# Performance work log

Measured on AMD Instinct MI355X. Metric: run time of the kernel, lower is better.

## Reference

```python
import jax, jax.numpy as jnp
import numpy as np

EPS = 1e-12  # F.normalize eps
NEG_SLOPE = 0.2


def setup_inputs() -> dict:
    key = jax.random.key(0)
    ks = jax.random.split(key, 12)
    n_users, n_items, d, nnz, B = 100000, 100000, 64, 6400000, 4096
    N = n_users + n_items
    return {
        "rows": jax.random.randint(ks[0], (nnz,), 0, N, dtype=jnp.int32),
        "cols": jax.random.randint(ks[1], (nnz,), 0, N, dtype=jnp.int32),
        "vals": jax.random.uniform(ks[2], (nnz,), dtype=jnp.float32),
        "user_emb": jax.random.normal(ks[3], (n_users, d), dtype=jnp.float32),
        "item_emb": jax.random.normal(ks[4], (n_items, d), dtype=jnp.float32),
        "W_gc": jax.random.normal(ks[5], (3, d, d), dtype=jnp.float32) * 0.1,
        "b_gc": jax.random.normal(ks[6], (3, 1, d), dtype=jnp.float32) * 0.1,
        "W_bi": jax.random.normal(ks[7], (3, d, d), dtype=jnp.float32) * 0.1,
        "b_bi": jax.random.normal(ks[8], (3, 1, d), dtype=jnp.float32) * 0.1,
        "u": jax.random.randint(ks[9], (B,), 0, n_users, dtype=jnp.int32),
        "i": jax.random.randint(ks[10], (B,), 0, n_items, dtype=jnp.int32),
        "j": jax.random.randint(ks[11], (B,), 0, n_items, dtype=jnp.int32),
    }


def reference(rows, cols, vals, user_emb, item_emb, W_gc, b_gc, W_bi, b_bi, u, i, j):
    n_users = user_emb.shape[0]
    N = n_users + item_emb.shape[0]
    ego = jnp.concatenate([user_emb, item_emb], axis=0)  # [N, d]
    all_embeddings = [ego]
    for k in range(W_gc.shape[0]):
        # sparse adjacency SpMM: side[r] = sum_e vals[e] * ego[cols[e]] for rows[e]==r
        side = jax.ops.segment_sum(vals[:, None] * ego[cols], rows, num_segments=N)
        sum_emb = side @ W_gc[k] + b_gc[k]
        bi_emb = (ego * side) @ W_bi[k] + b_bi[k]
        ego = jax.nn.leaky_relu(sum_emb + bi_emb, negative_slope=NEG_SLOPE)
        # dropout p=0 (eval) -> identity; L2 normalize per node
        norm = jnp.linalg.norm(ego, axis=1, keepdims=True)
        all_embeddings.append(ego / jnp.maximum(norm, EPS))
    all_embeddings = jnp.concatenate(all_embeddings, axis=1)  # [N, d*(L+1)]
    u_g = all_embeddings[:n_users][u]
    i_g = all_embeddings[n_users:]
    return u_g, i_g[i], i_g[j]
```

## Files before the change

kernel.cpp:

```cpp
#include <hip/hip_runtime.h>
#include <hip/hip_bf16.h>

#define D 64
#define NEG_SLOPE 0.2f
#define EPS 1e-12f
#define CB 9
#define CROWS (1 << CB)
#define NBC_MAX 1024
#define TILE_E 8192

__device__ __forceinline__ unsigned short f32_to_bf16(float f) {
  unsigned b = __float_as_uint(f);
  return (unsigned short)((b + 0x7FFF + ((b >> 16) & 1)) >> 16);
}


__global__ __launch_bounds__(256) void hist_coarse(const int* __restrict__ rows,
                                                   int* __restrict__ bcount,
                                                   int nnz, int nbc) {
  __shared__ int h[NBC_MAX];
  for (int i = threadIdx.x; i < nbc; i += 256) h[i] = 0;
  __syncthreads();
  for (int k = blockIdx.x * 256 + threadIdx.x; k < nnz; k += gridDim.x * 256)
    atomicAdd(&h[rows[k] >> CB], 1);
  __syncthreads();
  for (int i = threadIdx.x; i < nbc; i += 256)
    if (h[i]) atomicAdd(&bcount[i], h[i]);
}

#define SCAN_E2 4
__global__ __launch_bounds__(256) void scan_buckets(
    const int* __restrict__ bcount, int* __restrict__ bbase,
    int* __restrict__ bcursor, int nbc, int nnz, int* __restrict__ row_ptr,
    int N) {
  __shared__ int sums[256];
  int base = threadIdx.x * SCAN_E2;
  int c[SCAN_E2];
  int tsum = 0;
#pragma unroll
  for (int i = 0; i < SCAN_E2; i++) {
    int idx = base + i;
    c[i] = (idx < nbc) ? bcount[idx] : 0;
    tsum += c[i];
  }
  sums[threadIdx.x] = tsum;
  __syncthreads();
  for (int off = 1; off < 256; off <<= 1) {
    int t = (threadIdx.x >= off) ? sums[threadIdx.x - off] : 0;
    __syncthreads();
    sums[threadIdx.x] += t;
    __syncthreads();
  }
  int run = sums[threadIdx.x] - tsum;
#pragma unroll
  for (int i = 0; i < SCAN_E2; i++) {
    int idx = base + i;
    if (idx < nbc) {
      bbase[idx] = run;
      bcursor[idx] = run;
    }
    run += c[i];
  }
  if (threadIdx.x == 255) {
    bbase[nbc] = sums[255];
    row_ptr[N] = nnz;
  }
}

__global__ __launch_bounds__(256) void scatter_ranked(
    const int* __restrict__ rows, const int* __restrict__ cols,
    const float* __restrict__ vals, int* __restrict__ bcursor,
    int2* __restrict__ bucketed, int nnz, int nbc) {
  __shared__ int h[NBC_MAX];
  int ntiles = (nnz + TILE_E - 1) / TILE_E;
  for (int tile = blockIdx.x; tile < ntiles; tile += gridDim.x) {
    int s = tile * TILE_E;
    int e = min(s + TILE_E, nnz);
    for (int i = threadIdx.x; i < nbc; i += 256) h[i] = 0;
    __syncthreads();
    for (int k = s + threadIdx.x; k < e; k += 256)
      atomicAdd(&h[rows[k] >> CB], 1);
    __syncthreads();
    for (int i = threadIdx.x; i < nbc; i += 256) {
      int c = h[i];
      h[i] = c ? atomicAdd(&bcursor[i], c) : 0;
    }
    __syncthreads();
    for (int k = s + threadIdx.x; k < e; k += 256) {
      int r = rows[k];
      int pos = atomicAdd(&h[r >> CB], 1);
      bucketed[pos] =
          make_int2(cols[k] | ((r & (CROWS - 1)) << 20), __float_as_int(vals[k]));
    }
    __syncthreads();
  }
}

__global__ __launch_bounds__(256) void sort_csr(
    const int2* __restrict__ bucketed, const int* __restrict__ bbase,
    int* __restrict__ row_ptr, int2* __restrict__ pairs, int N) {
  __shared__ int lhist[CROWS];
  __shared__ int sums[256];
  int b = blockIdx.x;
  int s = bbase[b];
  int e = bbase[b + 1];
  int t = threadIdx.x;
  for (int i = t; i < CROWS; i += 256) lhist[i] = 0;
  __syncthreads();
  for (int k = s + t; k < e; k += 256)
    atomicAdd(&lhist[(unsigned)bucketed[k].x >> 20], 1);
  __syncthreads();
  int c0 = lhist[2 * t];
  int c1 = lhist[2 * t + 1];
  int tsum = c0 + c1;
  sums[t] = tsum;
  __syncthreads();
  for (int off = 1; off < 256; off <<= 1) {
    int v = (t >= off) ? sums[t - off] : 0;
    __syncthreads();
    sums[t] += v;
    __syncthreads();
  }
  int run = sums[t] - tsum;
  int base0 = s + run;
  int base1 = base0 + c0;
  lhist[2 * t] = base0;
  lhist[2 * t + 1] = base1;
  int grow = (b << CB) + 2 * t;
  if (grow < N) row_ptr[grow] = base0;
  if (grow + 1 < N) row_ptr[grow + 1] = base1;
  __syncthreads();
  for (int k = s + t; k < e; k += 256) {
    int2 g = bucketed[k];
    int lr = (unsigned)g.x >> 20;
    int dst = atomicAdd(&lhist[lr], 1);
    pairs[dst] = make_int2(g.x & 0xFFFFF, g.y);
  }
}

__global__ __launch_bounds__(256) void init_ego(
    const float* __restrict__ user_emb, const float* __restrict__ item_emb,
    float* __restrict__ ego, unsigned short* __restrict__ ego16,
    int nU4, int nT4, int w16) {
  int i = blockIdx.x * 256 + threadIdx.x;
  if (i >= nT4) return;
  float4 v = (i < nU4) ? ((const float4*)user_emb)[i]
                       : ((const float4*)item_emb)[i - nU4];
  ((float4*)ego)[i] = v;
  if (w16) {
    ushort4 o;
    o.x = f32_to_bf16(v.x);
    o.y = f32_to_bf16(v.y);
    o.z = f32_to_bf16(v.z);
    o.w = f32_to_bf16(v.w);
    ((ushort4*)ego16)[i] = o;
  }
}

__global__ __launch_bounds__(256) void spmm_gather_bf16(
    const int* __restrict__ row_ptr, const int2* __restrict__ pairs,
    const unsigned short* __restrict__ ego16, float* __restrict__ side, int N) {
  int wave = threadIdx.x >> 6;
  int lane = threadIdx.x & 63;
  int g = lane >> 4;
  int l = lane & 15;
  unsigned lofs = (unsigned)(l << 2);
  int w = blockIdx.x * 4 + wave;
  int stride = gridDim.x * 4;
  for (int n = w; n < N; n += stride) {
    int s = row_ptr[n];
    int e = row_ptr[n + 1];
    float a0 = 0.f, a1 = 0.f, a2 = 0.f, a3 = 0.f;
    float b0 = 0.f, b1 = 0.f, b2 = 0.f, b3 = 0.f;
    if (s < e) {
      int lim = e - 1;
      int2 p0 = pairs[min(s + g, lim)];
      int2 p1 = pairs[min(s + 4 + g, lim)];
      int2 p2 = pairs[min(s + 8 + g, lim)];
      int2 p3 = pairs[min(s + 12 + g, lim)];
      for (int k = s; k < e; k += 16) {
        unsigned o0 = ((unsigned)p0.x << 6) + lofs;
        unsigned o1 = ((unsigned)p1.x << 6) + lofs;
        unsigned o2 = ((unsigned)p2.x << 6) + lofs;
        unsigned o3 = ((unsigned)p3.x << 6) + lofs;
        ushort4 x0 = *(const ushort4*)(ego16 + o0);
        ushort4 x1 = *(const ushort4*)(ego16 + o1);
        ushort4 x2 = *(const ushort4*)(ego16 + o2);
        ushort4 x3 = *(const ushort4*)(ego16 + o3);
        int kn = k + 16;
        int2 q0 = pairs[min(kn + g, lim)];
        int2 q1 = pairs[min(kn + 4 + g, lim)];
        int2 q2 = pairs[min(kn + 8 + g, lim)];
        int2 q3 = pairs[min(kn + 12 + g, lim)];
        float v0 = (k + g < e) ? __int_as_float(p0.y) : 0.f;
        float v1 = (k + 4 + g < e) ? __int_as_float(p1.y) : 0.f;
        float v2 = (k + 8 + g < e) ? __int_as_float(p2.y) : 0.f;
        float v3 = (k + 12 + g < e) ? __int_as_float(p3.y) : 0.f;
        a0 = fmaf(v0, __uint_as_float((unsigned)x0.x << 16), a0);
        a1 = fmaf(v0, __uint_as_float((unsigned)x0.y << 16), a1);
        a2 = fmaf(v0, __uint_as_float((unsigned)x0.z << 16), a2);
        a3 = fmaf(v0, __uint_as_float((unsigned)x0.w << 16), a3);
        b0 = fmaf(v1, __uint_as_float((unsigned)x1.x << 16), b0);
        b1 = fmaf(v1, __uint_as_float((unsigned)x1.y << 16), b1);
        b2 = fmaf(v1, __uint_as_float((unsigned)x1.z << 16), b2);
        b3 = fmaf(v1, __uint_as_float((unsigned)x1.w << 16), b3);
        a0 = fmaf(v2, __uint_as_float((unsigned)x2.x << 16), a0);
        a1 = fmaf(v2, __uint_as_float((unsigned)x2.y << 16), a1);
        a2 = fmaf(v2, __uint_as_float((unsigned)x2.z << 16), a2);
        a3 = fmaf(v2, __uint_as_float((unsigned)x2.w << 16), a3);
        b0 = fmaf(v3, __uint_as_float((unsigned)x3.x << 16), b0);
        b1 = fmaf(v3, __uint_as_float((unsigned)x3.y << 16), b1);
        b2 = fmaf(v3, __uint_as_float((unsigned)x3.z << 16), b2);
        b3 = fmaf(v3, __uint_as_float((unsigned)x3.w << 16), b3);
        p0 = q0; p1 = q1; p2 = q2; p3 = q3;
      }
    }
    a0 += b0; a1 += b1; a2 += b2; a3 += b3;
    a0 += __shfl_xor(a0, 16);
    a1 += __shfl_xor(a1, 16);
    a2 += __shfl_xor(a2, 16);
    a3 += __shfl_xor(a3, 16);
    a0 += __shfl_xor(a0, 32);
    a1 += __shfl_xor(a1, 32);
    a2 += __shfl_xor(a2, 32);
    a3 += __shfl_xor(a3, 32);
    if (g == 0) {
      ((float4*)(side + ((size_t)n << 6)))[l] = make_float4(a0, a1, a2, a3);
    }
  }
}

__global__ __launch_bounds__(256) void spmm_gather_packed(
    const int* __restrict__ row_ptr, const int2* __restrict__ pairs,
    const float* __restrict__ ego, float* __restrict__ side, int N) {
  int wave = threadIdx.x >> 6;
  int lane = threadIdx.x & 63;
  int w = blockIdx.x * 4 + wave;
  int stride = gridDim.x * 4;
  for (int n = w; n < N; n += stride) {
    int s = row_ptr[n];
    int e = row_ptr[n + 1];
    float acc = 0.f;
    int k = s;
    for (; k + 3 < e; k += 4) {
      int2 p0 = pairs[k], p1 = pairs[k + 1], p2 = pairs[k + 2], p3 = pairs[k + 3];
      float x0 = ego[(size_t)p0.x * D + lane];
      float x1 = ego[(size_t)p1.x * D + lane];
      float x2 = ego[(size_t)p2.x * D + lane];
      float x3 = ego[(size_t)p3.x * D + lane];
      acc = fmaf(__int_as_float(p0.y), x0, acc);
      acc = fmaf(__int_as_float(p1.y), x1, acc);
      acc = fmaf(__int_as_float(p2.y), x2, acc);
      acc = fmaf(__int_as_float(p3.y), x3, acc);
    }
    for (; k < e; k++) {
      int2 p = pairs[k];
      acc = fmaf(__int_as_float(p.y), ego[(size_t)p.x * D + lane], acc);
    }
    side[(size_t)n * D + lane] = acc;
  }
}

__global__ __launch_bounds__(256) void scatter_spmm(
    const int* __restrict__ rows, const int* __restrict__ cols,
    const float* __restrict__ vals, const float* __restrict__ ego,
    float* __restrict__ side, int nnz) {
  long long t = (long long)blockIdx.x * blockDim.x + threadIdx.x;
  int e = (int)(t >> 4);
  if (e >= nnz) return;
  int c4 = (int)(t & 15);
  int r = rows[e];
  int c = cols[e];
  float v = vals[e];
  const float4* src = (const float4*)(ego + (size_t)c * D);
  float4 x = src[c4];
  float* dst = side + (size_t)r * D + c4 * 4;
  atomicAdd(dst + 0, v * x.x);
  atomicAdd(dst + 1, v * x.y);
  atomicAdd(dst + 2, v * x.z);
  atomicAdd(dst + 3, v * x.w);
}

__global__ __launch_bounds__(256, 2) void transform_nodes(
    float* __restrict__ ego, const float* __restrict__ side,
    const float* __restrict__ Wgc, const float* __restrict__ bgc,
    const float* __restrict__ Wbi, const float* __restrict__ bbi,
    unsigned short* __restrict__ ego16, int w16, int N) {
  __shared__ float sSP[4][2 * D];

  int wave = threadIdx.x >> 6;
  int lane = threadIdx.x & 63;

  float wg[D], wb[D];
#pragma unroll
  for (int i = 0; i < D; i++) {
    wg[i] = Wgc[i * D + lane];
    wb[i] = Wbi[i * D + lane];
  }
  float bg = bgc[lane];
  float bb = bbi[lane];

  int waveGlobal = blockIdx.x * 4 + wave;
  int nWaves = gridDim.x * 4;

  float2* spw = (float2*)sSP[wave];
  const float4* q = (const float4*)sSP[wave];

  int n = waveGlobal;
  float s = 0.f, e = 0.f;
  if (n < N) {
    s = side[(size_t)n * D + lane];
    e = ego[(size_t)n * D + lane];
  }
  for (; n < N; n += nWaves) {
    spw[lane] = make_float2(s, e * s);
    int nn = n + nWaves;
    float sN = 0.f, eN = 0.f;
    if (nn < N) {
      sN = side[(size_t)nn * D + lane];
      eN = ego[(size_t)nn * D + lane];
    }
    float ag0 = bg, ab0 = bb;
    float ag1 = 0.f, ab1 = 0.f, ag2 = 0.f, ab2 = 0.f, ag3 = 0.f, ab3 = 0.f;
#pragma unroll
    for (int j = 0; j < D / 2; j += 2) {
      float4 p0 = q[j];
      float4 p1 = q[j + 1];
      ag0 = fmaf(p0.x, wg[2 * j], ag0);
      ab0 = fmaf(p0.y, wb[2 * j], ab0);
      ag1 = fmaf(p0.z, wg[2 * j + 1], ag1);
      ab1 = fmaf(p0.w, wb[2 * j + 1], ab1);
      ag2 = fmaf(p1.x, wg[2 * j + 2], ag2);
      ab2 = fmaf(p1.y, wb[2 * j + 2], ab2);
      ag3 = fmaf(p1.z, wg[2 * j + 3], ag3);
      ab3 = fmaf(p1.w, wb[2 * j + 3], ab3);
    }
    float v = (ag0 + ag1 + ag2 + ag3) + (ab0 + ab1 + ab2 + ab3);
    v = v > 0.f ? v : NEG_SLOPE * v;
    ego[(size_t)n * D + lane] = v;
    if (w16) ego16[(size_t)n * D + lane] = f32_to_bf16(v);
    s = sN;
    e = eN;
  }
}

__global__ __launch_bounds__(256) void gather_out(
    const float* __restrict__ ego, const int* __restrict__ u,
    const int* __restrict__ iidx, const int* __restrict__ jidx,
    float* __restrict__ out, int n_users, int B, int slice, int normalize) {
  int r = blockIdx.x * 4 + (threadIdx.x >> 6);
  int lane = threadIdx.x & 63;
  if (r >= 3 * B) return;
  int which = r / B;
  int b = r - which * B;
  int n = (which == 0) ? u[b] : (n_users + ((which == 1) ? iidx[b] : jidx[b]));
  float v = ego[(size_t)n * D + lane];
  if (normalize) {
    float sq = v * v;
#pragma unroll
    for (int off = 32; off > 0; off >>= 1) sq += __shfl_xor(sq, off);
    float norm = sqrtf(sq);
    v = v / fmaxf(norm, EPS);
  }
  out[(size_t)which * B * 256 + (size_t)b * 256 + slice * D + lane] = v;
}

extern "C" void kernel_launch(void* const* d_in, const int* in_sizes, int n_in,
                              void* d_out, int out_size, void* d_ws, size_t ws_size,
                              hipStream_t stream) {
  const int*   rows     = (const int*)d_in[0];
  const int*   cols     = (const int*)d_in[1];
  const float* vals     = (const float*)d_in[2];
  const float* user_emb = (const float*)d_in[3];
  const float* item_emb = (const float*)d_in[4];
  const float* W_gc     = (const float*)d_in[5];
  const float* b_gc     = (const float*)d_in[6];
  const float* W_bi     = (const float*)d_in[7];
  const float* b_bi     = (const float*)d_in[8];
  const int*   u        = (const int*)d_in[9];
  const int*   iidx     = (const int*)d_in[10];
  const int*   jidx     = (const int*)d_in[11];

  int nnz     = in_sizes[0];
  int n_users = in_sizes[3] / D;
  int n_items = in_sizes[4] / D;
  int N       = n_users + n_items;
  int B       = in_sizes[9];
  float* out  = (float*)d_out;

  int nbc = (N + CROWS - 1) >> CB;

  auto align256 = [](size_t x) { return (x + 255) & ~(size_t)255; };
  char* p = (char*)d_ws;
  size_t egoBytes  = align256((size_t)N * D * sizeof(float));
  size_t sideBytes = align256((size_t)N * D * sizeof(float));
  if ((size_t)nnz * sizeof(int2) > sideBytes)
    sideBytes = align256((size_t)nnz * sizeof(int2));

  float* ego  = (float*)p; p += egoBytes;
  float* side = (float*)p;
  int2* bucketed = (int2*)side;
  p += sideBytes;
  int* row_ptr = (int*)p; p += align256((size_t)(N + 1) * sizeof(int));
  int* bcount  = (int*)p; p += align256((size_t)(nbc + 1) * sizeof(int));
  int* bbase   = (int*)p; p += align256((size_t)(nbc + 1) * sizeof(int));
  int* bcursor = (int*)p; p += align256((size_t)(nbc + 1) * sizeof(int));
  int2* pairs  = (int2*)p; p += align256((size_t)nnz * sizeof(int2));
  size_t need_csr = (size_t)(p - (char*)d_ws);
  unsigned short* ego16 = (unsigned short*)p;
  p += align256((size_t)N * D * sizeof(unsigned short));
  size_t need_16 = (size_t)(p - (char*)d_ws);

  int mode  = (ws_size >= need_csr && N <= (1 << 20) && nbc <= NBC_MAX) ? 0 : 2;
  int use16 = (mode == 0 && ws_size >= need_16) ? 1 : 0;

  int nU4 = n_users * D / 4;
  int nT4 = N * D / 4;
  init_ego<<<(nT4 + 255) / 256, 256, 0, stream>>>(user_emb, item_emb, ego,
                                                  ego16, nU4, nT4, use16);

  if (mode == 0) {
    hipMemsetAsync(bcount, 0, (size_t)nbc * sizeof(int), stream);
    hist_coarse<<<256, 256, 0, stream>>>(rows, bcount, nnz, nbc);
    scan_buckets<<<1, 256, 0, stream>>>(bcount, bbase, bcursor, nbc, nnz,
                                        row_ptr, N);
    int ntiles = (nnz + TILE_E - 1) / TILE_E;
    scatter_ranked<<<ntiles, 256, 0, stream>>>(rows, cols, vals, bcursor,
                                               bucketed, nnz, nbc);
    sort_csr<<<nbc, 256, 0, stream>>>(bucketed, bbase, row_ptr, pairs, N);
  }

  int gblocks = (3 * B + 3) / 4;
  gather_out<<<gblocks, 256, 0, stream>>>(ego, u, iidx, jidx, out, n_users, B,
                                          0, 0);

  long long sthreads = (long long)nnz * 16;
  int sblocks = (int)((sthreads + 255) / 256);

  for (int k = 0; k < 3; k++) {
    if (mode == 0) {
      if (use16)
        spmm_gather_bf16<<<2048, 256, 0, stream>>>(row_ptr, pairs, ego16, side,
                                                   N);
      else
        spmm_gather_packed<<<2048, 256, 0, stream>>>(row_ptr, pairs, ego, side,
                                                     N);
    } else {
      hipMemsetAsync(side, 0, (size_t)N * D * sizeof(float), stream);
      scatter_spmm<<<sblocks, 256, 0, stream>>>(rows, cols, vals, ego, side,
                                                nnz);
    }
    transform_nodes<<<2048, 256, 0, stream>>>(
        ego, side, W_gc + (size_t)k * D * D, b_gc + (size_t)k * D,
        W_bi + (size_t)k * D * D, b_bi + (size_t)k * D, ego16, use16, N);
    gather_out<<<gblocks, 256, 0, stream>>>(ego, u, iidx, jidx, out, n_users,
                                            B, k + 1, 1);
  }
}
```

Measured before the change: 1.076 ms.

## Drop pairs prefetch in SpMM gather, process two nodes per wave in transform

The bf16 SpMM gather loop no longer software-prefetches the next 16 pairs; it loads pairs and gathers embeddings within the same iteration, which lowers register pressure but exposes the load latency of the pairs. transform_nodes now handles two nodes per wave iteration with double shared staging buffers, so every LDS weight pass feeds two independent FMA chains. The gather grid is doubled to 4096 blocks. The per-thread register budget in transform grows and the stall on pairs loads in the gather may increase.

```diff
diff --git a/kernel.cpp b/kernel.cpp
--- a/kernel.cpp
+++ b/kernel.cpp
@@ -172,48 +172,41 @@
     int e = row_ptr[n + 1];
     float a0 = 0.f, a1 = 0.f, a2 = 0.f, a3 = 0.f;
     float b0 = 0.f, b1 = 0.f, b2 = 0.f, b3 = 0.f;
-    if (s < e) {
+    for (int k = s; k < e; k += 16) {
       int lim = e - 1;
-      int2 p0 = pairs[min(s + g, lim)];
-      int2 p1 = pairs[min(s + 4 + g, lim)];
-      int2 p2 = pairs[min(s + 8 + g, lim)];
-      int2 p3 = pairs[min(s + 12 + g, lim)];
-      for (int k = s; k < e; k += 16) {
-        unsigned o0 = ((unsigned)p0.x << 6) + lofs;
-        unsigned o1 = ((unsigned)p1.x << 6) + lofs;
-        unsigned o2 = ((unsigned)p2.x << 6) + lofs;
-        unsigned o3 = ((unsigned)p3.x << 6) + lofs;
-        ushort4 x0 = *(const ushort4*)(ego16 + o0);
-        ushort4 x1 = *(const ushort4*)(ego16 + o1);
-        ushort4 x2 = *(const ushort4*)(ego16 + o2);
-        ushort4 x3 = *(const ushort4*)(ego16 + o3);
-        int kn = k + 16;
-        int2 q0 = pairs[min(kn + g, lim)];
-        int2 q1 = pairs[min(kn + 4 + g, lim)];
-        int2 q2 = pairs[min(kn + 8 + g, lim)];
-        int2 q3 = pairs[min(kn + 12 + g, lim)];
-        float v0 = (k + g < e) ? __int_as_float(p0.y) : 0.f;
-        float v1 = (k + 4 + g < e) ? __int_as_float(p1.y) : 0.f;
-        float v2 = (k + 8 + g < e) ? __int_as_float(p2.y) : 0.f;
-        float v3 = (k + 12 + g < e) ? __int_as_float(p3.y) : 0.f;
-        a0 = fmaf(v0, __uint_as_float((unsigned)x0.x << 16), a0);
-        a1 = fmaf(v0, __uint_as_float((unsigned)x0.y << 16), a1);
-        a2 = fmaf(v0, __uint_as_float((unsigned)x0.z << 16), a2);
-        a3 = fmaf(v0, __uint_as_float((unsigned)x0.w << 16), a3);
-        b0 = fmaf(v1, __uint_as_float((unsigned)x1.x << 16), b0);
-        b1 = fmaf(v1, __uint_as_float((unsigned)x1.y << 16), b1);
-        b2 = fmaf(v1, __uint_as_float((unsigned)x1.z << 16), b2);
-        b3 = fmaf(v1, __uint_as_float((unsigned)x1.w << 16), b3);
-        a0 = fmaf(v2, __uint_as_float((unsigned)x2.x << 16), a0);
-        a1 = fmaf(v2, __uint_as_float((unsigned)x2.y << 16), a1);
-        a2 = fmaf(v2, __uint_as_float((unsigned)x2.z << 16), a2);
-        a3 = fmaf(v2, __uint_as_float((unsigned)x2.w << 16), a3);
-        b0 = fmaf(v3, __uint_as_float((unsigned)x3.x << 16), b0);
-        b1 = fmaf(v3, __uint_as_float((unsigned)x3.y << 16), b1);
-        b2 = fmaf(v3, __uint_as_float((unsigned)x3.z << 16), b2);
-        b3 = fmaf(v3, __uint_as_float((unsigned)x3.w << 16), b3);
-        p0 = q0; p1 = q1; p2 = q2; p3 = q3;
-      }
+      int k0 = k + g, k1 = k0 + 4, k2 = k0 + 8, k3 = k0 + 12;
+      int2 p0 = pairs[min(k0, lim)];
+      int2 p1 = pairs[min(k1, lim)];
+      int2 p2 = pairs[min(k2, lim)];
+      int2 p3 = pairs[min(k3, lim)];
+      unsigned o0 = ((unsigned)p0.x << 6) + lofs;
+      unsigned o1 = ((unsigned)p1.x << 6) + lofs;
+      unsigned o2 = ((unsigned)p2.x << 6) + lofs;
+      unsigned o3 = ((unsigned)p3.x << 6) + lofs;
+      ushort4 x0 = *(const ushort4*)(ego16 + o0);
+      ushort4 x1 = *(const ushort4*)(ego16 + o1);
+      ushort4 x2 = *(const ushort4*)(ego16 + o2);
+      ushort4 x3 = *(const ushort4*)(ego16 + o3);
+      float v0 = (k0 < e) ? __int_as_float(p0.y) : 0.f;
+      float v1 = (k1 < e) ? __int_as_float(p1.y) : 0.f;
+      float v2 = (k2 < e) ? __int_as_float(p2.y) : 0.f;
+      float v3 = (k3 < e) ? __int_as_float(p3.y) : 0.f;
+      a0 = fmaf(v0, __uint_as_float((unsigned)x0.x << 16), a0);
+      a1 = fmaf(v0, __uint_as_float((unsigned)x0.y << 16), a1);
+      a2 = fmaf(v0, __uint_as_float((unsigned)x0.z << 16), a2);
+      a3 = fmaf(v0, __uint_as_float((unsigned)x0.w << 16), a3);
+      b0 = fmaf(v1, __uint_as_float((unsigned)x1.x << 16), b0);
+      b1 = fmaf(v1, __uint_as_float((unsigned)x1.y << 16), b1);
+      b2 = fmaf(v1, __uint_as_float((unsigned)x1.z << 16), b2);
+      b3 = fmaf(v1, __uint_as_float((unsigned)x1.w << 16), b3);
+      a0 = fmaf(v2, __uint_as_float((unsigned)x2.x << 16), a0);
+      a1 = fmaf(v2, __uint_as_float((unsigned)x2.y << 16), a1);
+      a2 = fmaf(v2, __uint_as_float((unsigned)x2.z << 16), a2);
+      a3 = fmaf(v2, __uint_as_float((unsigned)x2.w << 16), a3);
+      b0 = fmaf(v3, __uint_as_float((unsigned)x3.x << 16), b0);
+      b1 = fmaf(v3, __uint_as_float((unsigned)x3.y << 16), b1);
+      b2 = fmaf(v3, __uint_as_float((unsigned)x3.z << 16), b2);
+      b3 = fmaf(v3, __uint_as_float((unsigned)x3.w << 16), b3);
     }
     a0 += b0; a1 += b1; a2 += b2; a3 += b3;
     a0 += __shfl_xor(a0, 16);
@@ -286,7 +279,7 @@
     const float* __restrict__ Wgc, const float* __restrict__ bgc,
     const float* __restrict__ Wbi, const float* __restrict__ bbi,
     unsigned short* __restrict__ ego16, int w16, int N) {
-  __shared__ float sSP[4][2 * D];
+  __shared__ float sSP[4][2][2 * D];
 
   int wave = threadIdx.x >> 6;
   int lane = threadIdx.x & 63;
@@ -303,29 +296,46 @@
   int waveGlobal = blockIdx.x * 4 + wave;
   int nWaves = gridDim.x * 4;
 
-  float2* spw = (float2*)sSP[wave];
-  const float4* q = (const float4*)sSP[wave];
-
-  int n = waveGlobal;
-  float s = 0.f, e = 0.f;
-  if (n < N) {
-    s = side[(size_t)n * D + lane];
-    e = ego[(size_t)n * D + lane];
-  }
-  for (; n < N; n += nWaves) {
-    spw[lane] = make_float2(s, e * s);
-    int nn = n + nWaves;
-    float sN = 0.f, eN = 0.f;
-    if (nn < N) {
-      sN = side[(size_t)nn * D + lane];
-      eN = ego[(size_t)nn * D + lane];
+  float2* sp0 = (float2*)sSP[wave][0];
+  float2* sp1 = (float2*)sSP[wave][1];
+  const float4* q0 = (const float4*)sSP[wave][0];
+  const float4* q1 = (const float4*)sSP[wave][1];
+
+  int n0 = waveGlobal * 2;
+  int step = nWaves * 2;
+  float s0 = 0.f, e0 = 0.f, s1 = 0.f, e1 = 0.f;
+  if (n0 < N) {
+    s0 = side[(size_t)n0 * D + lane];
+    e0 = ego[(size_t)n0 * D + lane];
+  }
+  if (n0 + 1 < N) {
+    s1 = side[(size_t)(n0 + 1) * D + lane];
+    e1 = ego[(size_t)(n0 + 1) * D + lane];
+  }
+  for (; n0 < N; n0 += step) {
+    int n1 = n0 + 1;
+    sp0[lane] = make_float2(s0, e0 * s0);
+    sp1[lane] = make_float2(s1, e1 * s1);
+    int m0 = n0 + step, m1 = m0 + 1;
+    float sN0 = 0.f, eN0 = 0.f, sN1 = 0.f, eN1 = 0.f;
+    if (m0 < N) {
+      sN0 = side[(size_t)m0 * D + lane];
+      eN0 = ego[(size_t)m0 * D + lane];
+    }
+    if (m1 < N) {
+      sN1 = side[(size_t)m1 * D + lane];
+      eN1 = ego[(size_t)m1 * D + lane];
     }
     float ag0 = bg, ab0 = bb;
     float ag1 = 0.f, ab1 = 0.f, ag2 = 0.f, ab2 = 0.f, ag3 = 0.f, ab3 = 0.f;
+    float cg0 = bg, cb0 = bb;
+    float cg1 = 0.f, cb1 = 0.f, cg2 = 0.f, cb2 = 0.f, cg3 = 0.f, cb3 = 0.f;
 #pragma unroll
     for (int j = 0; j < D / 2; j += 2) {
-      float4 p0 = q[j];
-      float4 p1 = q[j + 1];
+      float4 p0 = q0[j];
+      float4 p1 = q0[j + 1];
+      float4 r0 = q1[j];
+      float4 r1 = q1[j + 1];
       ag0 = fmaf(p0.x, wg[2 * j], ag0);
       ab0 = fmaf(p0.y, wb[2 * j], ab0);
       ag1 = fmaf(p0.z, wg[2 * j + 1], ag1);
@@ -334,13 +344,26 @@
       ab2 = fmaf(p1.y, wb[2 * j + 2], ab2);
       ag3 = fmaf(p1.z, wg[2 * j + 3], ag3);
       ab3 = fmaf(p1.w, wb[2 * j + 3], ab3);
-    }
-    float v = (ag0 + ag1 + ag2 + ag3) + (ab0 + ab1 + ab2 + ab3);
-    v = v > 0.f ? v : NEG_SLOPE * v;
-    ego[(size_t)n * D + lane] = v;
-    if (w16) ego16[(size_t)n * D + lane] = f32_to_bf16(v);
-    s = sN;
-    e = eN;
+      cg0 = fmaf(r0.x, wg[2 * j], cg0);
+      cb0 = fmaf(r0.y, wb[2 * j], cb0);
+      cg1 = fmaf(r0.z, wg[2 * j + 1], cg1);
+      cb1 = fmaf(r0.w, wb[2 * j + 1], cb1);
+      cg2 = fmaf(r1.x, wg[2 * j + 2], cg2);
+      cb2 = fmaf(r1.y, wb[2 * j + 2], cb2);
+      cg3 = fmaf(r1.z, wg[2 * j + 3], cg3);
+      cb3 = fmaf(r1.w, wb[2 * j + 3], cb3);
+    }
+    float v0 = (ag0 + ag1 + ag2 + ag3) + (ab0 + ab1 + ab2 + ab3);
+    v0 = v0 > 0.f ? v0 : NEG_SLOPE * v0;
+    ego[(size_t)n0 * D + lane] = v0;
+    if (w16) ego16[(size_t)n0 * D + lane] = f32_to_bf16(v0);
+    if (n1 < N) {
+      float v1 = (cg0 + cg1 + cg2 + cg3) + (cb0 + cb1 + cb2 + cb3);
+      v1 = v1 > 0.f ? v1 : NEG_SLOPE * v1;
+      ego[(size_t)n1 * D + lane] = v1;
+      if (w16) ego16[(size_t)n1 * D + lane] = f32_to_bf16(v1);
+    }
+    s0 = sN0; e0 = eN0; s1 = sN1; e1 = eN1;
   }
 }
 
@@ -440,10 +463,10 @@
   for (int k = 0; k < 3; k++) {
     if (mode == 0) {
       if (use16)
-        spmm_gather_bf16<<<2048, 256, 0, stream>>>(row_ptr, pairs, ego16, side,
+        spmm_gather_bf16<<<4096, 256, 0, stream>>>(row_ptr, pairs, ego16, side,
                                                    N);
       else
-        spmm_gather_packed<<<2048, 256, 0, stream>>>(row_ptr, pairs, ego, side,
+        spmm_gather_packed<<<4096, 256, 0, stream>>>(row_ptr, pairs, ego, side,
                                                      N);
     } else {
       hipMemsetAsync(side, 0, (size_t)N * D * sizeof(float), stream);
```

After: 1.466 ms. +36.2%, slower.
